# Performance work log

Measured on AMD Instinct MI355X. Metric: run time of the kernel, lower is better.

## Reference

```python
import jax, jax.numpy as jnp
import numpy as np

B, N, M = 2, 256, 256  # batch items, bboxes per item, feature dim (output_channel)
BLOCKS = 2             # graph_conv_block_num


def _conv2d(x, w, b):
    # x: [C,H,W], w: [O,I,kh,kw] -> [O,H,W], SAME padding, stride 1
    y = jax.lax.conv_general_dilated(x[None], w, (1, 1), 'SAME',
                                     dimension_numbers=('NCHW', 'OIHW', 'NCHW'))
    return y[0] + b[:, None, None]


def setup_inputs() -> dict:
    key = jax.random.key(0)
    ks = jax.random.split(key, 8)
    s = 0.02  # small init to keep activations tame through conv stack
    return {
        'edge_feats': jax.random.normal(ks[0], (B, N, N, 7), jnp.float32),
        'node_feats': jax.random.normal(ks[1], (B, N, M), jnp.float32),
        'adapter_w': jax.random.normal(ks[2], (M, 7, 1, 1), jnp.float32) * s,
        'adapter_b': jnp.zeros((M,), jnp.float32),
        'conv0_w': jax.random.normal(ks[3], (M, 3 * M, 3, 3), jnp.float32) * s,
        'conv0_b': jnp.zeros((M,), jnp.float32),
        'conv1_w': jax.random.normal(ks[4], (M, M, 3, 3), jnp.float32) * s,
        'conv1_b': jnp.zeros((M,), jnp.float32),
        'last_w': jax.random.normal(ks[5], (M, M, 3, 3), jnp.float32) * s,
        'last_b': jnp.zeros((M,), jnp.float32),
        'att_w': jax.random.normal(ks[6], (1, M, 1, 1), jnp.float32) * s,
        'att_b': jnp.zeros((1,), jnp.float32),
    }


def reference(edge_feats, node_feats, adapter_w, adapter_b, conv0_w, conv0_b,
              conv1_w, conv1_b, last_w, last_b, att_w, att_b):
    def one(e, n):
        # e: [N,N,7], n: [N,M]
        edge = _conv2d(jnp.transpose(e, (2, 0, 1)), adapter_w, adapter_b)  # [M,N,N]
        node = n
        for _ in range(BLOCKS):  # conv weights shared across blocks, as in torch
            nT = node.T  # [M,N]
            # channel layout at (i,j): [node_i | edge_ij | node_j]
            feat = jnp.concatenate([
                jnp.broadcast_to(nT[:, :, None], (M, N, N)),
                edge,
                jnp.broadcast_to(nT[:, None, :], (M, N, N)),
            ], axis=0)  # [3M,N,N]
            feat = jax.nn.relu(_conv2d(feat, conv0_w, conv0_b))
            feat = jax.nn.relu(_conv2d(feat, conv1_w, conv1_b))
            # edge attention: 1x1 conv -> leaky_relu -> softmax over j -> weighted sum
            att = jax.nn.leaky_relu(_conv2d(feat, att_w, att_b))   # [1,N,N]
            coeff = jax.nn.softmax(att, axis=-1)                   # softmax over last dim
            node = jnp.sum(coeff * feat, axis=-1).T                # [N,M]
            edge = jax.nn.relu(_conv2d(feat, last_w, last_b))      # [M,N,N]
        return node, jnp.transpose(edge, (1, 2, 0))  # [N,M], [N,N,M]
    return jax.vmap(one)(edge_feats, node_feats)
```

## Files before the change

kernel.cpp:

```cpp
#include <hip/hip_runtime.h>
#include <hip/hip_bf16.h>

typedef __hip_bfloat16 bf16;
typedef __attribute__((ext_vector_type(8))) short s16x8;
typedef __attribute__((ext_vector_type(4))) float f32x4;

__device__ __forceinline__ float b2f(bf16 x) { return __bfloat162float(x); }
__device__ __forceinline__ bf16 f2b(float x) { return __float2bfloat16(x); }

__device__ __forceinline__ void gld16(const void* g, void* l) {
  __builtin_amdgcn_global_load_lds((const __attribute__((address_space(1))) unsigned int*)g,
                                   (__attribute__((address_space(3))) unsigned int*)l,
                                   16, 0, 0);
}

#define BARRIER() do { asm volatile("" ::: "memory"); \
                       __builtin_amdgcn_s_barrier();  \
                       asm volatile("" ::: "memory"); } while (0)

__global__ __launch_bounds__(256) void fill_sentinel(float* out, int n) {
  int idx = blockIdx.x * 256 + threadIdx.x;
  if (idx < n) out[idx] = 100.0f;
}

__global__ __launch_bounds__(256) void zero_fill(bf16* z) {
  z[blockIdx.x * 256 + threadIdx.x] = f2b(0.f);
}

__global__ __launch_bounds__(256) void pack_w(const float* __restrict__ c0w,
                                              const float* __restrict__ c1w,
                                              const float* __restrict__ lw,
                                              bf16* wp0, bf16* wp1, bf16* wp2, bf16* wnp) {
  const int SEG = 9 * 256 * 256;
  int idx = blockIdx.x * 256 + threadIdx.x;
  if (idx < 3 * SEG) {
    int which = idx / SEG, r = idx % SEG;
    int s = r >> 16, o = (r >> 8) & 255, c = r & 255;
    int ky = s / 3, kx = s - 3 * ky;
    if (which == 0)      wp0[r] = f2b(c0w[(((size_t)o * 768 + 256 + c) * 3 + ky) * 3 + kx]);
    else if (which == 1) wp1[r] = f2b(c1w[(((size_t)o * 256 + c) * 3 + ky) * 3 + kx]);
    else                 wp2[r] = f2b(lw [(((size_t)o * 256 + c) * 3 + ky) * 3 + kx]);
  } else {
    int r = idx - 3 * SEG;
    int m = r & 255, c = (r >> 8) & 255, tt = r >> 16;
    int ot = tt % 3, t2 = (tt / 3) % 3, p = tt / 9;
    int ky, kx, cin;
    if (p == 0) { kx = t2; ky = ot; cin = c; }
    else        { ky = t2; kx = ot; cin = 512 + c; }
    wnp[r] = f2b(c0w[(((size_t)m * 768 + cin) * 3 + ky) * 3 + kx]);
  }
}

__global__ __launch_bounds__(256) void adapter_k(const float* __restrict__ e,
                                                 const float* __restrict__ aw,
                                                 const float* __restrict__ ab,
                                                 bf16* __restrict__ E) {
  int i = blockIdx.x;
  int m = threadIdx.x;
  __shared__ float se[256 * 7];
  const size_t rb = (size_t)i * (256 * 7);
  for (int idx = m; idx < 256 * 7; idx += 256) se[idx] = e[rb + idx];
  __syncthreads();
  float w[7];
#pragma unroll
  for (int c = 0; c < 7; ++c) w[c] = aw[m * 7 + c];
  float bias = ab[m];
  bf16* ob = E + (size_t)i * 65536 + m;
  for (int j = 0; j < 256; ++j) {
    const float* ej = se + j * 7;
    float a = bias;
#pragma unroll
    for (int c = 0; c < 7; ++c) a += w[c] * ej[c];
    ob[(size_t)j * 256] = f2b(a);
  }
}

template <typename T>
__global__ __launch_bounds__(256) void node_terms(const T* __restrict__ nd,
                                                  const bf16* __restrict__ wnp,
                                                  float* __restrict__ TT) {
  int bid = blockIdx.x;
  int chunk = bid & 63;
  int t = (bid >> 6) % 3;
  int p = bid / 192;
  int tid = threadIdx.x;
  __shared__ float snd[6][256];
  int pos0 = chunk * 4;
  for (int idx = tid; idx < 6 * 256; idx += 256) {
    int r = idx >> 8, c = idx & 255;
    int gp = pos0 - 1 + r;
    snd[r][c] = (gp >= 0 && gp < 256) ? (float)nd[(size_t)gp * 256 + c] : 0.f;
  }
  __syncthreads();
  float acc[4] = {0.f, 0.f, 0.f, 0.f};
  const bf16* wb = wnp + (size_t)((p * 3 + t) * 3) * 65536 + tid;
  for (int c = 0; c < 256; ++c) {
    float w0 = b2f(wb[(size_t)c * 256]);
    float w1 = b2f(wb[(size_t)(65536 + c * 256)]);
    float w2 = b2f(wb[(size_t)(2 * 65536 + c * 256)]);
#pragma unroll
    for (int ii = 0; ii < 4; ++ii)
      acc[ii] += w0 * snd[ii][c] + w1 * snd[ii + 1][c] + w2 * snd[ii + 2][c];
  }
  float* o = TT + (((size_t)(p * 3 + t) * 256 + pos0) * 256) + tid;
#pragma unroll
  for (int ii = 0; ii < 4; ++ii) o[(size_t)ii * 256] = acc[ii];
}

template <int EPI, int F32OUT>
__global__ __launch_bounds__(512, 1)
void conv3x3_k(const bf16* __restrict__ inb, const bf16* __restrict__ wpack,
               const float* __restrict__ bias, void* __restrict__ outv,
               const float* __restrict__ TT, const bf16* __restrict__ zrow) {
  __shared__ __align__(16) char lds[131072];
  const int bid = blockIdx.x;
  const int i = ((bid & 7) << 5) + (bid >> 3);
  const int tid = threadIdx.x;
  const int lane = tid & 63, wid = tid >> 6;
  const int wr = wid >> 2, wc = wid & 3;
  const int lo = lane & 15, hi = lane >> 4;
  const int xlane = tid >> 3;
  const int sw = ((tid & 7) ^ (xlane & 7)) << 3;

  const int gxk0 = (hi ^ (lo & 7)) << 4;
  const int gxk1 = ((4 + hi) ^ (lo & 7)) << 4;
  const int aJ0 = (wr * 64 + lo) * 128 + gxk0;
  const int aJ1 = (wr * 64 + lo) * 128 + gxk1;
  const int bBase = ((wc & 1) * 64 + lo) * 128 + 65536 + (wc >> 1) * 16384;
  const int bJ0 = bBase + gxk0;
  const int bJ1 = bBase + gxk1;

  f32x4 acc00[4][2], acc01[4][2], acc10[4][2], acc11[4][2];
  const f32x4 z = {0.f, 0.f, 0.f, 0.f};
#pragma unroll
  for (int mf = 0; mf < 4; ++mf)
#pragma unroll
    for (int nf = 0; nf < 2; ++nf) { acc00[mf][nf] = z; acc01[mf][nf] = z;
                                     acc10[mf][nf] = z; acc11[mf][nf] = z; }
  s16x8 afA[4][2], afB[4][2], bf0[2][2], bf1[2][2];

  const bf16* rows0 = (i >= 1)   ? inb + (size_t)(i - 1) * 65536 : zrow;
  const bf16* rows1 = inb + (size_t)i * 65536;
  const bf16* rows2 = (i <= 254) ? inb + (size_t)(i + 1) * 65536 : zrow;

  auto STAGE_IN = [&](int t, int half) {
    const int ky = t / 12, rem = t - ky * 12, kx = rem >> 2, cc = rem & 3;
    const bf16* rowp = (ky == 0) ? rows0 : (ky == 1 ? rows1 : rows2);
    const int par = t & 1;
#pragma unroll
    for (int r = 0; r < 2; ++r) {
      const int px = half * 128 + r * 64 + xlane;
      const int j = px + kx - 1;
      const bf16* src = (j >= 0 && j <= 255)
          ? rowp + ((size_t)j << 8) + cc * 64 + sw
          : zrow + sw;
      gld16(src, lds + par * 32768 + half * 16384 + ((r * 64 + wid * 8) << 7));
    }
  };
  auto STAGE_W = [&](int t, int half) {
    const int ky = t / 12, rem = t - ky * 12, kx = rem >> 2, cc = rem & 3;
    const int s = ky * 3 + kx;
    const int par = t & 1;
#pragma unroll
    for (int r = 0; r < 2; ++r) {
      const int oc = half * 128 + r * 64 + xlane;
      gld16(wpack + ((size_t)s << 16) + ((size_t)oc << 8) + cc * 64 + sw,
            lds + 65536 + par * 32768 + half * 16384 + ((r * 64 + wid * 8) << 7));
    }
  };
  auto LD_A = [&](int par, int mh, s16x8 (&dst)[4][2]) {
#pragma unroll
    for (int mf = 0; mf < 4; ++mf) {
      dst[mf][0] = *(const s16x8*)(lds + aJ0 + mf * 2048 + mh * 16384 + par * 32768);
      dst[mf][1] = *(const s16x8*)(lds + aJ1 + mf * 2048 + mh * 16384 + par * 32768);
    }
  };
  auto LD_B = [&](int par, int nh, s16x8 (&dst)[2][2]) {
#pragma unroll
    for (int nf = 0; nf < 2; ++nf) {
      dst[nf][0] = *(const s16x8*)(lds + bJ0 + nh * 4096 + nf * 2048 + par * 32768);
      dst[nf][1] = *(const s16x8*)(lds + bJ1 + nh * 4096 + nf * 2048 + par * 32768);
    }
  };

#define MMA_Q(ACC, AF, BFR)                                                   \
  __builtin_amdgcn_s_setprio(1);                                              \
  _Pragma("unroll") for (int kk = 0; kk < 2; ++kk)                            \
  _Pragma("unroll") for (int mf = 0; mf < 4; ++mf)                            \
  _Pragma("unroll") for (int nf = 0; nf < 2; ++nf)                            \
    ACC[mf][nf] = __builtin_amdgcn_mfma_f32_16x16x32_bf16(                    \
        AF[mf][kk], BFR[nf][kk], ACC[mf][nf], 0, 0, 0);                       \
  __builtin_amdgcn_s_setprio(0);

  STAGE_IN(0, 0); STAGE_IN(0, 1); STAGE_W(0, 0); STAGE_W(0, 1); STAGE_IN(1, 0);
  asm volatile("s_waitcnt vmcnt(2)" ::: "memory");
  BARRIER();

#pragma unroll 1
  for (int u = 0; u < 18; ++u) {
    const int t1 = 2 * u + 1, t2 = 2 * u + 2, t3 = 2 * u + 3;
    const bool full = (u < 17);
    LD_A(0, 0, afA); LD_B(0, 0, bf0);
    STAGE_IN(t1, 1); STAGE_W(t1, 0);
    BARRIER();
    MMA_Q(acc00, afA, bf0);
    BARRIER();
    LD_B(0, 1, bf1);
    STAGE_W(t1, 1);
    BARRIER();
    MMA_Q(acc01, afA, bf1);
    BARRIER();
    LD_A(0, 1, afB);
    if (full) STAGE_IN(t2, 0);
    BARRIER();
    MMA_Q(acc10, afB, bf0);
    BARRIER();
    MMA_Q(acc11, afB, bf1);
    if (full) asm volatile("s_waitcnt vmcnt(2)" ::: "memory");
    else      asm volatile("s_waitcnt vmcnt(0)" ::: "memory");
    BARRIER();
    LD_A(1, 0, afA); LD_B(1, 0, bf0);
    if (full) { STAGE_IN(t2, 1); STAGE_W(t2, 0); }
    BARRIER();
    MMA_Q(acc00, afA, bf0);
    BARRIER();
    LD_B(1, 1, bf1);
    if (full) STAGE_W(t2, 1);
    BARRIER();
    MMA_Q(acc01, afA, bf1);
    BARRIER();
    LD_A(1, 1, afB);
    if (full) STAGE_IN(t3, 0);
    BARRIER();
    MMA_Q(acc10, afB, bf0);
    BARRIER();
    MMA_Q(acc11, afB, bf1);
    if (full) asm volatile("s_waitcnt vmcnt(2)" ::: "memory");
    else      asm volatile("s_waitcnt vmcnt(0)" ::: "memory");
    BARRIER();
  }
#undef MMA_Q

  bf16* orow = (bf16*)outv + (size_t)i * 65536;
  float* orowf = (float*)outv + (size_t)i * 65536;
#define EPI_Q(ACC, MH, NH)                                                    \
  _Pragma("unroll") for (int mf = 0; mf < 4; ++mf) {                          \
    _Pragma("unroll") for (int nf = 0; nf < 2; ++nf) {                        \
      const int o = wc * 64 + NH * 32 + nf * 16 + lo;                         \
      const float bs = bias[o];                                               \
      float ni0 = 0.f, ni1 = 0.f, ni2 = 0.f;                                  \
      if (EPI) { const float* TI = TT + (size_t)i * 256 + o;                  \
        ni0 = TI[0]; ni1 = TI[65536]; ni2 = TI[2 * 65536]; }                  \
      _Pragma("unroll") for (int rr = 0; rr < 4; ++rr) {                      \
        const int j = MH * 128 + wr * 64 + mf * 16 + hi * 4 + rr;             \
        float v = ACC[mf][nf][rr] + bs;                                       \
        if (EPI) {                                                            \
          v += ni1 + (j > 0 ? ni0 : 0.f) + (j < 255 ? ni2 : 0.f);             \
          const float* TJ = TT + (size_t)3 * 65536 + (size_t)j * 256 + o;     \
          float nj0 = TJ[0], nj1 = TJ[65536], nj2 = TJ[2 * 65536];            \
          v += nj1 + (i > 0 ? nj0 : 0.f) + (i < 255 ? nj2 : 0.f); }           \
        v = fmaxf(v, 0.f);                                                    \
        if (F32OUT) orowf[(size_t)j * 256 + o] = v;                           \
        else        orow[(size_t)j * 256 + o] = f2b(v);                       \
      } } }
  EPI_Q(acc00, 0, 0); EPI_Q(acc01, 0, 1); EPI_Q(acc10, 1, 0); EPI_Q(acc11, 1, 1);
#undef EPI_Q
}

template <int F32OUT>
__global__ __launch_bounds__(256) void att_wsum(const bf16* __restrict__ feat,
                                                const float* __restrict__ aw,
                                                const float* __restrict__ ab,
                                                bf16* __restrict__ ndb,
                                                float* __restrict__ ndf) {
  int i = blockIdx.x;
  int tid = threadIdx.x, lane = tid & 63, w = tid >> 6;
  __shared__ float s_aw[256];
  __shared__ float s_att[256];
  __shared__ float s_red[8];
  s_aw[tid] = aw[tid];
  __syncthreads();
  float a0 = s_aw[lane * 4], a1 = s_aw[lane * 4 + 1];
  float a2 = s_aw[lane * 4 + 2], a3 = s_aw[lane * 4 + 3];
  const bf16* fb = feat + (size_t)i * 65536;
  float abv = ab[0];
  for (int jj = 0; jj < 64; ++jj) {
    int j = w * 64 + jj;
    const bf16* f = fb + (size_t)j * 256 + lane * 4;
    float v = a0 * b2f(f[0]) + a1 * b2f(f[1]) + a2 * b2f(f[2]) + a3 * b2f(f[3]);
#pragma unroll
    for (int mk = 32; mk; mk >>= 1) v += __shfl_xor(v, mk);
    if (lane == 0) { float a = v + abv; s_att[j] = a > 0.f ? a : 0.01f * a; }
  }
  __syncthreads();
  float x = s_att[tid];
  float mx = x;
#pragma unroll
  for (int mk = 32; mk; mk >>= 1) mx = fmaxf(mx, __shfl_xor(mx, mk));
  if (lane == 0) s_red[w] = mx;
  __syncthreads();
  mx = fmaxf(fmaxf(s_red[0], s_red[1]), fmaxf(s_red[2], s_red[3]));
  float e = expf(x - mx);
  float sm = e;
#pragma unroll
  for (int mk = 32; mk; mk >>= 1) sm += __shfl_xor(sm, mk);
  if (lane == 0) s_red[4 + w] = sm;
  __syncthreads();
  sm = s_red[4] + s_red[5] + s_red[6] + s_red[7];
  __syncthreads();
  s_att[tid] = e / sm;
  __syncthreads();
  float acc = 0.f;
  for (int j = 0; j < 256; ++j) acc += s_att[j] * b2f(fb[(size_t)j * 256 + tid]);
  if (F32OUT) ndf[(size_t)i * 256 + tid] = acc;
  else        ndb[(size_t)i * 256 + tid] = f2b(acc);
}

extern "C" void kernel_launch(void* const* d_in, const int* in_sizes, int n_in,
                              void* d_out, int out_size, void* d_ws, size_t ws_size,
                              hipStream_t stream) {
  const float* edge_feats = (const float*)d_in[0];
  const float* node_feats = (const float*)d_in[1];
  const float* adapter_w  = (const float*)d_in[2];
  const float* adapter_b  = (const float*)d_in[3];
  const float* conv0_w    = (const float*)d_in[4];
  const float* conv0_b    = (const float*)d_in[5];
  const float* conv1_w    = (const float*)d_in[6];
  const float* conv1_b    = (const float*)d_in[7];
  const float* last_w     = (const float*)d_in[8];
  const float* last_b     = (const float*)d_in[9];
  const float* att_w      = (const float*)d_in[10];
  const float* att_b      = (const float*)d_in[11];
  float* out = (float*)d_out;

  char* ws = (char*)d_ws;
  size_t off = 0;
  bf16* Q    = (bf16*)(ws + off); off += (size_t)256 * 256 * 256 * 2;
  bf16* WP0  = (bf16*)(ws + off); off += (size_t)9 * 65536 * 2;
  bf16* WP1  = (bf16*)(ws + off); off += (size_t)9 * 65536 * 2;
  bf16* WP2  = (bf16*)(ws + off); off += (size_t)9 * 65536 * 2;
  bf16* WNP  = (bf16*)(ws + off); off += (size_t)18 * 65536 * 2;
  float* TT  = (float*)(ws + off); off += (size_t)2 * 3 * 65536 * 4;
  bf16* ND   = (bf16*)(ws + off); off += (size_t)65536 * 2;
  bf16* ZROW = (bf16*)(ws + off); off += (size_t)65536 * 2;
  if (ws_size < off) {
    fill_sentinel<<<(out_size + 255) / 256, 256, 0, stream>>>(out, out_size);
    return;
  }

  zero_fill<<<256, 256, 0, stream>>>(ZROW);
  pack_w<<<11520, 256, 0, stream>>>(conv0_w, conv1_w, last_w, WP0, WP1, WP2, WNP);

  for (int b = 0; b < 2; ++b) {
    bf16* P = (bf16*)(out + 131072 + (size_t)b * 16777216);
    float* edge_out = out + 131072 + (size_t)b * 16777216;
    float* node_out = out + (size_t)b * 65536;
    const float* eb = edge_feats + (size_t)b * 458752;
    const float* nb = node_feats + (size_t)b * 65536;

    adapter_k<<<256, 256, 0, stream>>>(eb, adapter_w, adapter_b, P);
    node_terms<float><<<384, 256, 0, stream>>>(nb, WNP, TT);
    conv3x3_k<1, 0><<<256, 512, 0, stream>>>(P, WP0, conv0_b, Q, TT, ZROW);
    conv3x3_k<0, 0><<<256, 512, 0, stream>>>(Q, WP1, conv1_b, P, nullptr, ZROW);
    att_wsum<0><<<256, 256, 0, stream>>>(P, att_w, att_b, ND, nullptr);
    conv3x3_k<0, 0><<<256, 512, 0, stream>>>(P, WP2, last_b, Q, nullptr, ZROW);
    node_terms<bf16><<<384, 256, 0, stream>>>(ND, WNP, TT);
    conv3x3_k<1, 0><<<256, 512, 0, stream>>>(Q, WP0, conv0_b, P, TT, ZROW);
    conv3x3_k<0, 0><<<256, 512, 0, stream>>>(P, WP1, conv1_b, Q, nullptr, ZROW);
    att_wsum<1><<<256, 256, 0, stream>>>(Q, att_w, att_b, nullptr, node_out);
    conv3x3_k<0, 1><<<256, 512, 0, stream>>>(Q, WP2, last_b, edge_out, nullptr, ZROW);
  }
}
```

Measured before the change: 1.229 ms.

## Replace direct global-to-LDS loads with register-staged prefetch and simplified K loop

Drops the global_load_lds async copies and the fine-grained multi-barrier schedule. Each K step now loads the next input and weight tiles into registers, runs all four MFMA quadrants from LDS, then writes the registers to the other LDS buffer with a single barrier per step. This cuts barrier count and control complexity, but adds register pressure, VGPR-to-LDS write traffic, and full vmcnt(0) waits that may expose memory latency.

```diff
diff --git a/kernel.cpp b/kernel.cpp
--- a/kernel.cpp
+++ b/kernel.cpp
@@ -7,12 +7,6 @@
 
 __device__ __forceinline__ float b2f(bf16 x) { return __bfloat162float(x); }
 __device__ __forceinline__ bf16 f2b(float x) { return __float2bfloat16(x); }
-
-__device__ __forceinline__ void gld16(const void* g, void* l) {
-  __builtin_amdgcn_global_load_lds((const __attribute__((address_space(1))) unsigned int*)g,
-                                   (__attribute__((address_space(3))) unsigned int*)l,
-                                   16, 0, 0);
-}
 
 #define BARRIER() do { asm volatile("" ::: "memory"); \
                        __builtin_amdgcn_s_barrier();  \
@@ -121,6 +115,7 @@
   const int lo = lane & 15, hi = lane >> 4;
   const int xlane = tid >> 3;
   const int sw = ((tid & 7) ^ (xlane & 7)) << 3;
+  const int g16 = (tid & 7) << 4;
 
   const int gxk0 = (hi ^ (lo & 7)) << 4;
   const int gxk1 = ((4 + hi) ^ (lo & 7)) << 4;
@@ -137,42 +132,44 @@
 #pragma unroll
     for (int nf = 0; nf < 2; ++nf) { acc00[mf][nf] = z; acc01[mf][nf] = z;
                                      acc10[mf][nf] = z; acc11[mf][nf] = z; }
-  s16x8 afA[4][2], afB[4][2], bf0[2][2], bf1[2][2];
+  s16x8 afA[4][2], bf0[2][2], bf1[2][2];
+  s16x8 gi[4], gw[4];
 
   const bf16* rows0 = (i >= 1)   ? inb + (size_t)(i - 1) * 65536 : zrow;
   const bf16* rows1 = inb + (size_t)i * 65536;
   const bf16* rows2 = (i <= 254) ? inb + (size_t)(i + 1) * 65536 : zrow;
 
-  auto STAGE_IN = [&](int t, int half) {
-    const int ky = t / 12, rem = t - ky * 12, kx = rem >> 2, cc = rem & 3;
+  auto ISSUE = [&](int t) {
+    const int ky = (t >= 24) ? 2 : ((t >= 12) ? 1 : 0);
+    const int rem = t - ky * 12;
+    const int kx = rem >> 2, cc = rem & 3;
     const bf16* rowp = (ky == 0) ? rows0 : (ky == 1 ? rows1 : rows2);
-    const int par = t & 1;
-#pragma unroll
-    for (int r = 0; r < 2; ++r) {
-      const int px = half * 128 + r * 64 + xlane;
+    const int s = ky * 3 + kx;
+#pragma unroll
+    for (int r = 0; r < 4; ++r) {
+      const int px = r * 64 + xlane;
       const int j = px + kx - 1;
       const bf16* src = (j >= 0 && j <= 255)
           ? rowp + ((size_t)j << 8) + cc * 64 + sw
           : zrow + sw;
-      gld16(src, lds + par * 32768 + half * 16384 + ((r * 64 + wid * 8) << 7));
+      gi[r] = *(const s16x8*)src;
+      gw[r] = *(const s16x8*)(wpack + ((size_t)s << 16) +
+                              (((size_t)(r * 64 + xlane)) << 8) + cc * 64 + sw);
     }
   };
-  auto STAGE_W = [&](int t, int half) {
-    const int ky = t / 12, rem = t - ky * 12, kx = rem >> 2, cc = rem & 3;
-    const int s = ky * 3 + kx;
-    const int par = t & 1;
-#pragma unroll
-    for (int r = 0; r < 2; ++r) {
-      const int oc = half * 128 + r * 64 + xlane;
-      gld16(wpack + ((size_t)s << 16) + ((size_t)oc << 8) + cc * 64 + sw,
-            lds + 65536 + par * 32768 + half * 16384 + ((r * 64 + wid * 8) << 7));
+  auto WRITE_STAGE = [&](int par) {
+#pragma unroll
+    for (int r = 0; r < 4; ++r) {
+      const int px = r * 64 + xlane;
+      *(s16x8*)(lds + par * 32768 + px * 128 + g16) = gi[r];
+      *(s16x8*)(lds + 65536 + par * 32768 + px * 128 + g16) = gw[r];
     }
   };
-  auto LD_A = [&](int par, int mh, s16x8 (&dst)[4][2]) {
+  auto LD_A = [&](int par, int mh) {
 #pragma unroll
     for (int mf = 0; mf < 4; ++mf) {
-      dst[mf][0] = *(const s16x8*)(lds + aJ0 + mf * 2048 + mh * 16384 + par * 32768);
-      dst[mf][1] = *(const s16x8*)(lds + aJ1 + mf * 2048 + mh * 16384 + par * 32768);
+      afA[mf][0] = *(const s16x8*)(lds + aJ0 + mf * 2048 + mh * 16384 + par * 32768);
+      afA[mf][1] = *(const s16x8*)(lds + aJ1 + mf * 2048 + mh * 16384 + par * 32768);
     }
   };
   auto LD_B = [&](int par, int nh, s16x8 (&dst)[2][2]) {
@@ -183,60 +180,36 @@
     }
   };
 
-#define MMA_Q(ACC, AF, BFR)                                                   \
+#define MMA_Q(ACC, BFR)                                                       \
   __builtin_amdgcn_s_setprio(1);                                              \
   _Pragma("unroll") for (int kk = 0; kk < 2; ++kk)                            \
   _Pragma("unroll") for (int mf = 0; mf < 4; ++mf)                            \
   _Pragma("unroll") for (int nf = 0; nf < 2; ++nf)                            \
     ACC[mf][nf] = __builtin_amdgcn_mfma_f32_16x16x32_bf16(                    \
-        AF[mf][kk], BFR[nf][kk], ACC[mf][nf], 0, 0, 0);                       \
+        afA[mf][kk], BFR[nf][kk], ACC[mf][nf], 0, 0, 0);                      \
   __builtin_amdgcn_s_setprio(0);
 
-  STAGE_IN(0, 0); STAGE_IN(0, 1); STAGE_W(0, 0); STAGE_W(0, 1); STAGE_IN(1, 0);
-  asm volatile("s_waitcnt vmcnt(2)" ::: "memory");
+  ISSUE(0);
+  asm volatile("s_waitcnt vmcnt(0)" ::: "memory");
+  WRITE_STAGE(0);
+  asm volatile("s_waitcnt lgkmcnt(0)" ::: "memory");
   BARRIER();
 
 #pragma unroll 1
-  for (int u = 0; u < 18; ++u) {
-    const int t1 = 2 * u + 1, t2 = 2 * u + 2, t3 = 2 * u + 3;
-    const bool full = (u < 17);
-    LD_A(0, 0, afA); LD_B(0, 0, bf0);
-    STAGE_IN(t1, 1); STAGE_W(t1, 0);
-    BARRIER();
-    MMA_Q(acc00, afA, bf0);
-    BARRIER();
-    LD_B(0, 1, bf1);
-    STAGE_W(t1, 1);
-    BARRIER();
-    MMA_Q(acc01, afA, bf1);
-    BARRIER();
-    LD_A(0, 1, afB);
-    if (full) STAGE_IN(t2, 0);
-    BARRIER();
-    MMA_Q(acc10, afB, bf0);
-    BARRIER();
-    MMA_Q(acc11, afB, bf1);
-    if (full) asm volatile("s_waitcnt vmcnt(2)" ::: "memory");
-    else      asm volatile("s_waitcnt vmcnt(0)" ::: "memory");
-    BARRIER();
-    LD_A(1, 0, afA); LD_B(1, 0, bf0);
-    if (full) { STAGE_IN(t2, 1); STAGE_W(t2, 0); }
-    BARRIER();
-    MMA_Q(acc00, afA, bf0);
-    BARRIER();
-    LD_B(1, 1, bf1);
-    if (full) STAGE_W(t2, 1);
-    BARRIER();
-    MMA_Q(acc01, afA, bf1);
-    BARRIER();
-    LD_A(1, 1, afB);
-    if (full) STAGE_IN(t3, 0);
-    BARRIER();
-    MMA_Q(acc10, afB, bf0);
-    BARRIER();
-    MMA_Q(acc11, afB, bf1);
-    if (full) asm volatile("s_waitcnt vmcnt(2)" ::: "memory");
-    else      asm volatile("s_waitcnt vmcnt(0)" ::: "memory");
+  for (int t = 0; t < 36; ++t) {
+    const int p = t & 1;
+    if (t < 35) ISSUE(t + 1);
+    LD_A(p, 0); LD_B(p, 0, bf0); LD_B(p, 1, bf1);
+    MMA_Q(acc00, bf0);
+    MMA_Q(acc01, bf1);
+    LD_A(p, 1);
+    MMA_Q(acc10, bf0);
+    MMA_Q(acc11, bf1);
+    if (t < 35) {
+      asm volatile("s_waitcnt vmcnt(0)" ::: "memory");
+      WRITE_STAGE(p ^ 1);
+    }
+    asm volatile("s_waitcnt lgkmcnt(0)" ::: "memory");
     BARRIER();
   }
 #undef MMA_Q
```

Result: no change. 1.253 ms (+1.9%).
